# Optimization experiments

Measured on AMD Instinct MI355X. Metric: run time of the kernel, lower is better.

The kernel has to match this reference:

```python
import jax, jax.numpy as jnp
import numpy as np

B, H, S, DK = 2, 16, 2048, 64
NEG = -1000000000.0

def setup_inputs() -> dict:
    key = jax.random.key(0)
    k1, k2, k3, k4 = jax.random.split(key, 4)
    Q = jax.random.normal(k1, (B, H, S, DK), dtype=jnp.float32)
    K = jax.random.normal(k2, (B, H, S, DK), dtype=jnp.float32)
    V = jax.random.normal(k3, (B, H, S, DK), dtype=jnp.float32)
    mask = jax.random.randint(k4, (B, 1, S, S), 0, 2).astype(bool)
    return {"Q": Q, "K": K, "V": V, "mask": mask}

def reference(Q, K, V, mask):
    sqrt_dk = jnp.asarray(DK ** 0.5, Q.dtype)
    # [B,H,S,S] scores, materialized as in the original module
    score = jnp.einsum('bhqd,bhkd->bhqk', Q, K) / sqrt_dk
    score = jnp.where(mask, jnp.asarray(NEG, score.dtype), score)
    attn_prob = jax.nn.softmax(score, axis=-1)  # dropout p=0.0 -> identity
    context = jnp.einsum('bhqk,bhkd->bhqd', attn_prob, V)
    return (context, attn_prob)
```

## Files before the change

kernel.cpp:

```cpp
#include <hip/hip_runtime.h>

static constexpr int Bc  = 2;
static constexpr int Hc  = 16;
static constexpr int Sc  = 2048;
static constexpr int DKc = 64;
static constexpr float SC2  = 0.18033688011112043f;

typedef __attribute__((ext_vector_type(8)))  short short8v;
typedef __attribute__((ext_vector_type(16))) float f32x16;
typedef __attribute__((ext_vector_type(4)))  float f32x4;

__device__ __forceinline__ unsigned short f2bf(float f) {
    union { float f; unsigned u; } v; v.f = f;
    unsigned r = v.u + 0x7FFFu + ((v.u >> 16) & 1u);
    return (unsigned short)(r >> 16);
}
__device__ __forceinline__ unsigned cvtpk(float lo, float hi) {
    unsigned r;
    asm("v_cvt_pk_bf16_f32 %0, %1, %2" : "=v"(r) : "v"(lo), "v"(hi));
    return r;
}
__device__ __forceinline__ float fexp2(float x) {
    float r;
    asm("v_exp_f32 %0, %1" : "=v"(r) : "v"(x));
    return r;
}
__device__ __forceinline__ float bflo(unsigned u) {
    union { unsigned u; float f; } v; v.u = u << 16; return v.f;
}
__device__ __forceinline__ float bfhi(unsigned u) {
    union { unsigned u; float f; } v; v.u = u & 0xFFFF0000u; return v.f;
}

__global__ void kfrag_kernel(const float* __restrict__ K, unsigned short* __restrict__ Kf) {
    int i = blockIdx.x * 256 + threadIdx.x;
    int lane = i & 63, ks = (i >> 6) & 3, t = (i >> 8) & 63, bh = i >> 14;
    int hi = lane >> 5, l31 = lane & 31;
    const float* src = K + (((size_t)bh * Sc + t * 32 + l31) * DKc + ks * 16 + hi * 8);
    float4 a = *(const float4*)src;
    float4 c = *(const float4*)(src + 4);
    short8v s;
    s[0]=(short)f2bf(a.x); s[1]=(short)f2bf(a.y); s[2]=(short)f2bf(a.z); s[3]=(short)f2bf(a.w);
    s[4]=(short)f2bf(c.x); s[5]=(short)f2bf(c.y); s[6]=(short)f2bf(c.z); s[7]=(short)f2bf(c.w);
    *(short8v*)&Kf[(size_t)i * 8] = s;
}

__global__ void vfrag_kernel(const float* __restrict__ V, unsigned short* __restrict__ Vf) {
    int i = blockIdx.x * 256 + threadIdx.x;
    int lane = i & 63, dblk = (i >> 6) & 1, ks = (i >> 7) & 1, t = (i >> 8) & 63, bh = i >> 14;
    int hi = lane >> 5, l31 = lane & 31;
    int k0 = t * 32 + ks * 16 + hi * 8, d = dblk * 32 + l31;
    const float* vb = V + ((size_t)bh * Sc + k0) * DKc + d;
    short8v s;
    #pragma unroll
    for (int u = 0; u < 8; ++u) s[u] = (short)f2bf(vb[(size_t)u * DKc]);
    *(short8v*)&Vf[(size_t)i * 8] = s;
}

__global__ void mfrag_kernel(const int* __restrict__ M, unsigned* __restrict__ Mf) {
    int w = blockIdx.x * 4 + (threadIdx.x >> 6);
    int lane = threadIdx.x & 63;
    const int* row = M + (size_t)w * Sc;
    int b = w >> 11, q = w & 2047, qt = q >> 5, r = q & 31;
    unsigned* ob = Mf + (size_t)(b * 64 + qt) * 2048 + r;
    for (int tp = 0; tp < 32; ++tp) {
        unsigned long long bal = __ballot(row[tp * 64 + lane] != 0);
        if (lane == 0)  ob[(size_t)(2 * tp)     * 32] = (unsigned)bal;
        if (lane == 32) ob[(size_t)(2 * tp + 1) * 32] = (unsigned)(bal >> 32);
    }
}

__global__ __launch_bounds__(256, 2)
void attn_main(const float* __restrict__ Q, const unsigned short* __restrict__ Kf,
               const unsigned short* __restrict__ Vf, const unsigned* __restrict__ Mf,
               float* __restrict__ out)
{
    const int wg  = (int)blockIdx.x;
    const int swz = (wg & 7) * 256 + (wg >> 3);
    const int bh  = swz >> 6;
    const int qt  = swz & 63;
    const int qb  = qt << 5;
    const int b   = bh >> 4;

    const int tid  = (int)threadIdx.x;
    const int wid  = tid >> 6;
    const int lane = tid & 63;
    const int hi   = lane >> 5;
    const int l31  = lane & 31;

    __shared__ float lbuf[4][32];
    __shared__ float lfin[32];
    __shared__ char  sbuf[2][32768];

    const unsigned short* kfb = Kf + (size_t)bh * 131072;
    const unsigned short* vfb = Vf + (size_t)bh * 131072;
    const unsigned*       mfb = Mf + (size_t)(b * 64 + qt) * 2048;

    short8v qf[4];
    {
        const float* qrow = Q + ((size_t)bh * Sc + qb + l31) * DKc;
        #pragma unroll
        for (int ks = 0; ks < 4; ++ks) {
            const float* p0 = qrow + ks * 16 + hi * 8;
            float4 a = *(const float4*)p0;
            float4 c = *(const float4*)(p0 + 4);
            short8v f;
            f[0]=(short)f2bf(a.x); f[1]=(short)f2bf(a.y); f[2]=(short)f2bf(a.z); f[3]=(short)f2bf(a.w);
            f[4]=(short)f2bf(c.x); f[5]=(short)f2bf(c.y); f[6]=(short)f2bf(c.z); f[7]=(short)f2bf(c.w);
            qf[ks] = f;
        }
    }

    f32x16 acc0, acc1;
    #pragma unroll
    for (int u = 0; u < 16; ++u) { acc0[u] = 0.0f; acc1[u] = 0.0f; }

    unsigned ec[16][8];
    float l_run = 0.0f;

    auto ldk = [&](int i, short8v* k4, unsigned& mw) {
        const int t = i * 4 + wid;
        #pragma unroll
        for (int ks = 0; ks < 4; ++ks)
            k4[ks] = *(const short8v*)&kfb[((size_t)(t * 4 + ks) * 64 + lane) * 8];
        mw = mfb[t * 32 + l31] >> (4 * hi);
    };

    auto body = [&](int i, const short8v* k4, unsigned mw) {
        const int t = i * 4 + wid;
        f32x16 sc;
        #pragma unroll
        for (int u = 0; u < 16; ++u) sc[u] = 0.0f;
        #pragma unroll
        for (int ks = 0; ks < 4; ++ks)
            sc = __builtin_amdgcn_mfma_f32_32x32x16_bf16(k4[ks], qf[ks], sc, 0, 0, 0);

        short8v v0 = *(const short8v*)&vfb[((size_t)(t * 4 + 0) * 64 + lane) * 8];
        short8v v1 = *(const short8v*)&vfb[((size_t)(t * 4 + 1) * 64 + lane) * 8];

        #pragma unroll
        for (int g = 0; g < 4; ++g)
            #pragma unroll
            for (int j = 0; j < 4; ++j) {
                float a = sc[4*g+j] * SC2;
                a = ((mw >> (8*g + j)) & 1u) ? -1e30f : a;
                sc[4*g+j] = fexp2(a);
            }

        float ps = 0.0f;
        #pragma unroll
        for (int u = 0; u < 16; ++u) ps += sc[u];
        ps += __shfl_xor(ps, 32);
        l_run += ps;

        #pragma unroll
        for (int g = 0; g < 4; ++g) {
            ec[i][2*g]   = cvtpk(sc[4*g],   sc[4*g+1]);
            ec[i][2*g+1] = cvtpk(sc[4*g+2], sc[4*g+3]);
        }

        #pragma unroll
        for (int ks = 0; ks < 2; ++ks) {
            if (ks == 1) {
                v0 = *(const short8v*)&vfb[((size_t)(t * 4 + 2) * 64 + lane) * 8];
                v1 = *(const short8v*)&vfb[((size_t)(t * 4 + 3) * 64 + lane) * 8];
            }
            unsigned o0x = ec[i][4*ks], o0y = ec[i][4*ks+1];
            unsigned o1x = ec[i][4*ks+2], o1y = ec[i][4*ks+3];
            unsigned s0x = __shfl_xor(o0x, 32), s0y = __shfl_xor(o0y, 32);
            unsigned s1x = __shfl_xor(o1x, 32), s1y = __shfl_xor(o1y, 32);
            union { unsigned u[4]; short8v s; } pa;
            pa.u[0] = hi ? s1x : o0x;
            pa.u[1] = hi ? s1y : o0y;
            pa.u[2] = hi ? o1x : s0x;
            pa.u[3] = hi ? o1y : s0y;
            acc0 = __builtin_amdgcn_mfma_f32_32x32x16_bf16(pa.s, v0, acc0, 0, 0, 0);
            acc1 = __builtin_amdgcn_mfma_f32_32x32x16_bf16(pa.s, v1, acc1, 0, 0, 0);
        }
    };

    short8v kA[4], kB[4];
    unsigned mwA, mwB;
    ldk(0, kA, mwA);
    #pragma unroll
    for (int i = 0; i < 16; i += 2) {
        ldk(i + 1, kB, mwB);
        body(i, kA, mwA);
        if (i + 2 < 16) ldk(i + 2, kA, mwA);
        body(i + 1, kB, mwB);
    }

    if (hi == 0) lbuf[wid][l31] = l_run;
    __syncthreads();
    if (tid < 32) lfin[tid] = lbuf[0][tid] + lbuf[1][tid] + lbuf[2][tid] + lbuf[3][tid];
    __syncthreads();
    const float inv_l = 1.0f / lfin[l31];

    float* ctx   = out;
    float* attn  = out + (size_t)Bc * Hc * Sc * DKc;
    float* prow0 = attn + ((size_t)bh * Sc + qb) * Sc;

    #pragma unroll
    for (int r = 0; r < 8; ++r) {
        char* sb = &sbuf[r & 1][0];
        #pragma unroll
        for (int sub = 0; sub < 2; ++sub) {
            const int i = r * 2 + sub;
            #pragma unroll
            for (int g = 0; g < 4; ++g) {
                unsigned u0 = ec[i][2*g], u1 = ec[i][2*g+1];
                f32x4 st;
                st.x = bflo(u0) * inv_l; st.y = bfhi(u0) * inv_l;
                st.z = bflo(u1) * inv_l; st.w = bfhi(u1) * inv_l;
                *(f32x4*)(sb + sub * 16384 + l31 * 512 +
                          ((wid * 128 + 32*g + 16*hi) ^ ((l31 & 7) << 4))) = st;
            }
        }
        __syncthreads();
        #pragma unroll
        for (int j = 0; j < 8; ++j) {
            const int row = j * 4 + wid;
            f32x4 ld = *(const f32x4*)(&sbuf[r & 1][0] + (lane >> 5) * 16384 + row * 512 +
                                       (((lane & 31) * 16) ^ ((row & 7) << 4)));
            __builtin_nontemporal_store(ld, (f32x4*)(prow0 + (size_t)row * Sc + r * 256 + lane * 4));
        }
    }

    __syncthreads();
    float* pall = (float*)&sbuf[0][0];
    if (wid >= 2) {
        #pragma unroll
        for (int g = 0; g < 4; ++g)
            #pragma unroll
            for (int j = 0; j < 4; ++j) {
                int row = 8*g + 4*hi + j;
                pall[(wid - 2) * 2048 + row * 64 + l31]      = acc0[4*g+j];
                pall[(wid - 2) * 2048 + row * 64 + l31 + 32] = acc1[4*g+j];
            }
    }
    __syncthreads();
    if (wid < 2) {
        #pragma unroll
        for (int g = 0; g < 4; ++g)
            #pragma unroll
            for (int j = 0; j < 4; ++j) {
                int row = 8*g + 4*hi + j;
                acc0[4*g+j] += pall[wid * 2048 + row * 64 + l31];
                acc1[4*g+j] += pall[wid * 2048 + row * 64 + l31 + 32];
            }
    }
    __syncthreads();
    if (wid == 1) {
        #pragma unroll
        for (int g = 0; g < 4; ++g)
            #pragma unroll
            for (int j = 0; j < 4; ++j) {
                int row = 8*g + 4*hi + j;
                pall[row * 64 + l31]      = acc0[4*g+j];
                pall[row * 64 + l31 + 32] = acc1[4*g+j];
            }
    }
    __syncthreads();
    if (wid == 0) {
        #pragma unroll
        for (int g = 0; g < 4; ++g)
            #pragma unroll
            for (int j = 0; j < 4; ++j) {
                int row = 8*g + 4*hi + j;
                float rinv = 1.0f / lfin[row];
                float o0 = (acc0[4*g+j] + pall[row * 64 + l31])      * rinv;
                float o1 = (acc1[4*g+j] + pall[row * 64 + l31 + 32]) * rinv;
                size_t off = ((size_t)bh * Sc + qb + row) * DKc + l31;
                ctx[off]      = o0;
                ctx[off + 32] = o1;
            }
    }
}

extern "C" void kernel_launch(void* const* d_in, const int* in_sizes, int n_in,
                              void* d_out, int out_size, void* d_ws, size_t ws_size,
                              hipStream_t stream)
{
    const float* Q = (const float*)d_in[0];
    const float* K = (const float*)d_in[1];
    const float* V = (const float*)d_in[2];
    const int*   M = (const int*)d_in[3];
    float* out = (float*)d_out;

    unsigned short* Kf = (unsigned short*)d_ws;
    unsigned short* Vf = (unsigned short*)((char*)d_ws + (8u << 20));
    unsigned*       Mf = (unsigned*)((char*)d_ws + (16u << 20));

    hipLaunchKernelGGL(kfrag_kernel, dim3(2048), dim3(256), 0, stream, K, Kf);
    hipLaunchKernelGGL(vfrag_kernel, dim3(2048), dim3(256), 0, stream, V, Vf);
    hipLaunchKernelGGL(mfrag_kernel, dim3(1024), dim3(256), 0, stream, M, Mf);
    hipLaunchKernelGGL(attn_main,    dim3(2048), dim3(256), 0, stream, Q, Kf, Vf, Mf, out);
}
```

Before: 184.3 us.

## Process four query tiles per workgroup, overlapping attn stores with next tile compute

Each workgroup now handles four consecutive 32-row query tiles instead of one, so the grid shrinks from 2048 to 512 workgroups. The attention-probability write-out of the previous tile is interleaved with the QK/softmax/PV compute of the next tile, aiming to hide the large global store traffic behind MFMA work. This costs parallelism, since 512 workgroups may underfill the GPU at two per CU. It also adds extra barriers inside the loop and makes the last tile's store phase serial.

```diff
diff --git a/kernel.cpp b/kernel.cpp
--- a/kernel.cpp
+++ b/kernel.cpp
@@ -75,12 +75,11 @@
                const unsigned short* __restrict__ Vf, const unsigned* __restrict__ Mf,
                float* __restrict__ out)
 {
-    const int wg  = (int)blockIdx.x;
-    const int swz = (wg & 7) * 256 + (wg >> 3);
-    const int bh  = swz >> 6;
-    const int qt  = swz & 63;
-    const int qb  = qt << 5;
-    const int b   = bh >> 4;
+    const int wg   = (int)blockIdx.x;
+    const int swz  = (wg & 7) * 64 + (wg >> 3);
+    const int bh   = swz >> 4;
+    const int quad = swz & 15;
+    const int b    = bh >> 4;
 
     const int tid  = (int)threadIdx.x;
     const int wid  = tid >> 6;
@@ -94,10 +93,17 @@
 
     const unsigned short* kfb = Kf + (size_t)bh * 131072;
     const unsigned short* vfb = Vf + (size_t)bh * 131072;
-    const unsigned*       mfb = Mf + (size_t)(b * 64 + qt) * 2048;
-
-    short8v qf[4];
-    {
+
+    float* ctx  = out;
+    float* attn = out + (size_t)Bc * Hc * Sc * DKc;
+
+    short8v  qf[4];
+    unsigned ec[16][8];
+    f32x16   acc0, acc1;
+    float    l_run;
+    const unsigned* mfb = nullptr;
+
+    auto loadqf = [&](int qb) {
         const float* qrow = Q + ((size_t)bh * Sc + qb + l31) * DKc;
         #pragma unroll
         for (int ks = 0; ks < 4; ++ks) {
@@ -109,16 +115,9 @@
             f[4]=(short)f2bf(c.x); f[5]=(short)f2bf(c.y); f[6]=(short)f2bf(c.z); f[7]=(short)f2bf(c.w);
             qf[ks] = f;
         }
-    }
-
-    f32x16 acc0, acc1;
-    #pragma unroll
-    for (int u = 0; u < 16; ++u) { acc0[u] = 0.0f; acc1[u] = 0.0f; }
-
-    unsigned ec[16][8];
-    float l_run = 0.0f;
-
-    auto ldk = [&](int i, short8v* k4, unsigned& mw) {
+    };
+
+    auto bodyLoad = [&](int i, short8v* k4, unsigned& mw) {
         const int t = i * 4 + wid;
         #pragma unroll
         for (int ks = 0; ks < 4; ++ks)
@@ -126,7 +125,7 @@
         mw = mfb[t * 32 + l31] >> (4 * hi);
     };
 
-    auto body = [&](int i, const short8v* k4, unsigned mw) {
+    auto bodyCompute = [&](int i, const short8v* k4, unsigned mw) {
         const int t = i * 4 + wid;
         f32x16 sc;
         #pragma unroll
@@ -179,30 +178,7 @@
         }
     };
 
-    short8v kA[4], kB[4];
-    unsigned mwA, mwB;
-    ldk(0, kA, mwA);
-    #pragma unroll
-    for (int i = 0; i < 16; i += 2) {
-        ldk(i + 1, kB, mwB);
-        body(i, kA, mwA);
-        if (i + 2 < 16) ldk(i + 2, kA, mwA);
-        body(i + 1, kB, mwB);
-    }
-
-    if (hi == 0) lbuf[wid][l31] = l_run;
-    __syncthreads();
-    if (tid < 32) lfin[tid] = lbuf[0][tid] + lbuf[1][tid] + lbuf[2][tid] + lbuf[3][tid];
-    __syncthreads();
-    const float inv_l = 1.0f / lfin[l31];
-
-    float* ctx   = out;
-    float* attn  = out + (size_t)Bc * Hc * Sc * DKc;
-    float* prow0 = attn + ((size_t)bh * Sc + qb) * Sc;
-
-    #pragma unroll
-    for (int r = 0; r < 8; ++r) {
-        char* sb = &sbuf[r & 1][0];
+    auto stage = [&](int r, char* sb, float inv) {
         #pragma unroll
         for (int sub = 0; sub < 2; ++sub) {
             const int i = r * 2 + sub;
@@ -210,70 +186,131 @@
             for (int g = 0; g < 4; ++g) {
                 unsigned u0 = ec[i][2*g], u1 = ec[i][2*g+1];
                 f32x4 st;
-                st.x = bflo(u0) * inv_l; st.y = bfhi(u0) * inv_l;
-                st.z = bflo(u1) * inv_l; st.w = bfhi(u1) * inv_l;
+                st.x = bflo(u0) * inv; st.y = bfhi(u0) * inv;
+                st.z = bflo(u1) * inv; st.w = bfhi(u1) * inv;
                 *(f32x4*)(sb + sub * 16384 + l31 * 512 +
                           ((wid * 128 + 32*g + 16*hi) ^ ((l31 & 7) << 4))) = st;
             }
         }
-        __syncthreads();
+    };
+
+    auto storeRound = [&](int r, const char* sb, float* prow) {
         #pragma unroll
         for (int j = 0; j < 8; ++j) {
             const int row = j * 4 + wid;
-            f32x4 ld = *(const f32x4*)(&sbuf[r & 1][0] + (lane >> 5) * 16384 + row * 512 +
+            f32x4 ld = *(const f32x4*)(sb + (lane >> 5) * 16384 + row * 512 +
                                        (((lane & 31) * 16) ^ ((row & 7) << 4)));
-            __builtin_nontemporal_store(ld, (f32x4*)(prow0 + (size_t)row * Sc + r * 256 + lane * 4));
-        }
+            __builtin_nontemporal_store(ld, (f32x4*)(prow + (size_t)row * Sc + r * 256 + lane * 4));
+        }
+    };
+
+    auto lfinalize = [&]() {
+        if (hi == 0) lbuf[wid][l31] = l_run;
+        __syncthreads();
+        if (tid < 32) lfin[tid] = lbuf[0][tid] + lbuf[1][tid] + lbuf[2][tid] + lbuf[3][tid];
+        __syncthreads();
+    };
+
+    auto octx = [&](int qb) {
+        float* pall = (float*)&sbuf[0][0];
+        if (wid >= 2) {
+            #pragma unroll
+            for (int g = 0; g < 4; ++g)
+                #pragma unroll
+                for (int j = 0; j < 4; ++j) {
+                    int row = 8*g + 4*hi + j;
+                    pall[(wid - 2) * 2048 + row * 64 + l31]      = acc0[4*g+j];
+                    pall[(wid - 2) * 2048 + row * 64 + l31 + 32] = acc1[4*g+j];
+                }
+        }
+        __syncthreads();
+        if (wid < 2) {
+            #pragma unroll
+            for (int g = 0; g < 4; ++g)
+                #pragma unroll
+                for (int j = 0; j < 4; ++j) {
+                    int row = 8*g + 4*hi + j;
+                    acc0[4*g+j] += pall[wid * 2048 + row * 64 + l31];
+                    acc1[4*g+j] += pall[wid * 2048 + row * 64 + l31 + 32];
+                }
+        }
+        __syncthreads();
+        if (wid == 1) {
+            #pragma unroll
+            for (int g = 0; g < 4; ++g)
+                #pragma unroll
+                for (int j = 0; j < 4; ++j) {
+                    int row = 8*g + 4*hi + j;
+                    pall[row * 64 + l31]      = acc0[4*g+j];
+                    pall[row * 64 + l31 + 32] = acc1[4*g+j];
+                }
+        }
+        __syncthreads();
+        if (wid == 0) {
+            #pragma unroll
+            for (int g = 0; g < 4; ++g)
+                #pragma unroll
+                for (int j = 0; j < 4; ++j) {
+                    int row = 8*g + 4*hi + j;
+                    float rinv = 1.0f / lfin[row];
+                    float o0 = (acc0[4*g+j] + pall[row * 64 + l31])      * rinv;
+                    float o1 = (acc1[4*g+j] + pall[row * 64 + l31 + 32]) * rinv;
+                    size_t off = ((size_t)bh * Sc + qb + row) * DKc + l31;
+                    ctx[off]      = o0;
+                    ctx[off + 32] = o1;
+                }
+        }
+    };
+
+    int qb = quad * 128;
+    mfb = Mf + (size_t)(b * 64 + quad * 4) * 2048;
+    loadqf(qb);
+    l_run = 0.0f;
+    #pragma unroll
+    for (int u = 0; u < 16; ++u) { acc0[u] = 0.0f; acc1[u] = 0.0f; }
+    #pragma unroll
+    for (int i = 0; i < 16; ++i) {
+        short8v k4[4]; unsigned mw;
+        bodyLoad(i, k4, mw);
+        bodyCompute(i, k4, mw);
     }
+    lfinalize();
+    float inv_prev = 1.0f / lfin[l31];
+    octx(qb);
+    float* prow_prev = attn + ((size_t)bh * Sc + qb) * Sc;
+
+    for (int tt = 1; tt < 4; ++tt) {
+        __syncthreads();
+        qb = quad * 128 + tt * 32;
+        mfb = Mf + (size_t)(b * 64 + quad * 4 + tt) * 2048;
+        loadqf(qb);
+        l_run = 0.0f;
+        #pragma unroll
+        for (int u = 0; u < 16; ++u) { acc0[u] = 0.0f; acc1[u] = 0.0f; }
+
+        #pragma unroll
+        for (int r = 0; r < 8; ++r) {
+            stage(r, &sbuf[r & 1][0], inv_prev);
+            __syncthreads();
+            short8v kA[4]; unsigned mA;
+            bodyLoad(2 * r, kA, mA);
+            storeRound(r, &sbuf[r & 1][0], prow_prev);
+            bodyCompute(2 * r, kA, mA);
+            bodyLoad(2 * r + 1, kA, mA);
+            bodyCompute(2 * r + 1, kA, mA);
+        }
+        lfinalize();
+        inv_prev = 1.0f / lfin[l31];
+        octx(qb);
+        prow_prev = attn + ((size_t)bh * Sc + qb) * Sc;
+    }
 
     __syncthreads();
-    float* pall = (float*)&sbuf[0][0];
-    if (wid >= 2) {
-        #pragma unroll
-        for (int g = 0; g < 4; ++g)
-            #pragma unroll
-            for (int j = 0; j < 4; ++j) {
-                int row = 8*g + 4*hi + j;
-                pall[(wid - 2) * 2048 + row * 64 + l31]      = acc0[4*g+j];
-                pall[(wid - 2) * 2048 + row * 64 + l31 + 32] = acc1[4*g+j];
-            }
-    }
-    __syncthreads();
-    if (wid < 2) {
-        #pragma unroll
-        for (int g = 0; g < 4; ++g)
-            #pragma unroll
-            for (int j = 0; j < 4; ++j) {
-                int row = 8*g + 4*hi + j;
-                acc0[4*g+j] += pall[wid * 2048 + row * 64 + l31];
-                acc1[4*g+j] += pall[wid * 2048 + row * 64 + l31 + 32];
-            }
-    }
-    __syncthreads();
-    if (wid == 1) {
-        #pragma unroll
-        for (int g = 0; g < 4; ++g)
-            #pragma unroll
-            for (int j = 0; j < 4; ++j) {
-                int row = 8*g + 4*hi + j;
-                pall[row * 64 + l31]      = acc0[4*g+j];
-                pall[row * 64 + l31 + 32] = acc1[4*g+j];
-            }
-    }
-    __syncthreads();
-    if (wid == 0) {
-        #pragma unroll
-        for (int g = 0; g < 4; ++g)
-            #pragma unroll
-            for (int j = 0; j < 4; ++j) {
-                int row = 8*g + 4*hi + j;
-                float rinv = 1.0f / lfin[row];
-                float o0 = (acc0[4*g+j] + pall[row * 64 + l31])      * rinv;
-                float o1 = (acc1[4*g+j] + pall[row * 64 + l31 + 32]) * rinv;
-                size_t off = ((size_t)bh * Sc + qb + row) * DKc + l31;
-                ctx[off]      = o0;
-                ctx[off + 32] = o1;
-            }
+    #pragma unroll
+    for (int r = 0; r < 8; ++r) {
+        stage(r, &sbuf[r & 1][0], inv_prev);
+        __syncthreads();
+        storeRound(r, &sbuf[r & 1][0], prow_prev);
     }
 }
 
@@ -294,5 +331,5 @@
     hipLaunchKernelGGL(kfrag_kernel, dim3(2048), dim3(256), 0, stream, K, Kf);
     hipLaunchKernelGGL(vfrag_kernel, dim3(2048), dim3(256), 0, stream, V, Vf);
     hipLaunchKernelGGL(mfrag_kernel, dim3(1024), dim3(256), 0, stream, M, Mf);
-    hipLaunchKernelGGL(attn_main,    dim3(2048), dim3(256), 0, stream, Q, Kf, Vf, Mf, out);
-}
+    hipLaunchKernelGGL(attn_main,    dim3(512),  dim3(256), 0, stream, Q, Kf, Vf, Mf, out);
+}
```

After: 361.0 us. 95.9% more time.
